# Performance work log

Hardware: AMD Instinct MI355X
Metric: run time of the kernel (lower is better)

Reference implementation:

```python
import jax, jax.numpy as jnp
import numpy as np

L, H, FF, NH = 6, 1024, 4096, 8
HD = H // NH
B, S = 4, 1024
EPS = 1e-5


def _fp8_roundtrip(w):
    # matches torch path: cast to float8_e4m3fn and back (done once at init, no grad)
    return w.astype(jnp.float8_e4m3fn).astype(w.dtype)


def setup_inputs() -> dict:
    key = jax.random.key(0)
    ks = jax.random.split(key, 6)
    x = jax.random.normal(ks[0], (B, S, H), dtype=jnp.float32)
    sH = 1.0 / np.sqrt(H)
    sF = 1.0 / np.sqrt(FF)
    qkv_w = _fp8_roundtrip(jax.random.normal(ks[1], (L, 3 * H, H), jnp.float32) * sH)
    proj_w = _fp8_roundtrip(jax.random.normal(ks[2], (L, H, H), jnp.float32) * sH)
    fc1_w = _fp8_roundtrip(jax.random.normal(ks[3], (L, FF, H), jnp.float32) * sH)
    fc2_w = _fp8_roundtrip(jax.random.normal(ks[4], (L, H, FF), jnp.float32) * sF)
    return {
        "x": x,
        "qkv_w": qkv_w, "qkv_b": jnp.zeros((L, 3 * H), jnp.float32),
        "proj_w": proj_w, "proj_b": jnp.zeros((L, H), jnp.float32),
        "fc1_w": fc1_w, "fc1_b": jnp.zeros((L, FF), jnp.float32),
        "fc2_w": fc2_w, "fc2_b": jnp.zeros((L, H), jnp.float32),
        "ln1_s": jnp.ones((L, H), jnp.float32), "ln1_b": jnp.zeros((L, H), jnp.float32),
        "ln2_s": jnp.ones((L, H), jnp.float32), "ln2_b": jnp.zeros((L, H), jnp.float32),
    }


def _layernorm(x, scale, bias):
    mu = jnp.mean(x, axis=-1, keepdims=True)
    var = jnp.var(x, axis=-1, keepdims=True)
    return (x - mu) / jnp.sqrt(var + EPS) * scale + bias


def reference(x, qkv_w, qkv_b, proj_w, proj_b, fc1_w, fc1_b, fc2_w, fc2_b,
              ln1_s, ln1_b, ln2_s, ln2_b):
    b, s, h = x.shape
    for i in range(L):
        # --- attention block ---
        residual = x
        hx = _layernorm(x, ln1_s[i], ln1_b[i])
        qkv = hx @ qkv_w[i].T + qkv_b[i]                       # [b, s, 3h]
        q, k, v = jnp.split(qkv, 3, axis=-1)
        q = q.reshape(b, s, NH, HD).transpose(0, 2, 1, 3)      # [b, nh, s, hd]
        k = k.reshape(b, s, NH, HD).transpose(0, 2, 1, 3)
        v = v.reshape(b, s, NH, HD).transpose(0, 2, 1, 3)
        scores = jnp.einsum('bhqd,bhkd->bhqk', q, k) / np.sqrt(HD)
        attn = jax.nn.softmax(scores, axis=-1)
        out = jnp.einsum('bhqk,bhkd->bhqd', attn, v)           # [b, nh, s, hd]
        out = out.transpose(0, 2, 1, 3).reshape(b, s, h)
        x = out @ proj_w[i].T + proj_b[i] + residual
        # --- FFN block ---
        residual = x
        hx = _layernorm(x, ln2_s[i], ln2_b[i])
        ff = jax.nn.relu(hx @ fc1_w[i].T + fc1_b[i])
        x = ff @ fc2_w[i].T + fc2_b[i] + residual
    return x
```

## Files before the change

kernel.cpp:

```cpp
#include <hip/hip_runtime.h>
#include <stdint.h>

typedef __bf16 bf16;
typedef __bf16 bf16x4 __attribute__((ext_vector_type(4)));
typedef __bf16 bf16x8 __attribute__((ext_vector_type(8)));
typedef float  f32x4  __attribute__((ext_vector_type(4)));

#define NLAYER 6
#define HDIM   1024
#define FFDIM  4096
#define NHEAD  8
#define HEADD  128
#define SEQ    1024
#define NTOK   4096

__device__ __forceinline__ void g2l16(const void* g, void* l) {
  __builtin_amdgcn_global_load_lds(
      (const __attribute__((address_space(1))) void*)g,
      (__attribute__((address_space(3))) void*)l, 16, 0, 0);
}

__global__ __launch_bounds__(256) void cvt_w(const float* __restrict__ in,
                                             bf16* __restrict__ out, int n8) {
  int i = blockIdx.x * 256 + threadIdx.x;
  if (i >= n8) return;
  const f32x4* p = (const f32x4*)in + (size_t)i * 2;
  f32x4 a = p[0], b = p[1];
  bf16x8 o;
  o[0] = (bf16)a[0]; o[1] = (bf16)a[1]; o[2] = (bf16)a[2]; o[3] = (bf16)a[3];
  o[4] = (bf16)b[0]; o[5] = (bf16)b[1]; o[6] = (bf16)b[2]; o[7] = (bf16)b[3];
  *((bf16x8*)out + i) = o;
}

__global__ __launch_bounds__(256) void ln_k(const float* __restrict__ x,
                                            const float* __restrict__ sc,
                                            const float* __restrict__ bi,
                                            bf16* __restrict__ out) {
  int row = blockIdx.x, t = threadIdx.x;
  f32x4 v = *((const f32x4*)(x + (size_t)row * HDIM) + t);
  float s = v[0] + v[1] + v[2] + v[3];
  float q = v[0]*v[0] + v[1]*v[1] + v[2]*v[2] + v[3]*v[3];
#pragma unroll
  for (int m = 1; m < 64; m <<= 1) {
    s += __shfl_xor(s, m, 64);
    q += __shfl_xor(q, m, 64);
  }
  __shared__ float ss[4], qq[4];
  if ((t & 63) == 0) { ss[t >> 6] = s; qq[t >> 6] = q; }
  __syncthreads();
  s = ss[0] + ss[1] + ss[2] + ss[3];
  q = qq[0] + qq[1] + qq[2] + qq[3];
  float mu  = s * (1.f / HDIM);
  float var = q * (1.f / HDIM) - mu * mu;
  float rs  = rsqrtf(var + 1e-5f);
  f32x4 g = *((const f32x4*)sc + t);
  f32x4 b = *((const f32x4*)bi + t);
  bf16x4 o;
#pragma unroll
  for (int j = 0; j < 4; j++) o[j] = (bf16)((v[j] - mu) * rs * g[j] + b[j]);
  *((bf16x4*)(out + (size_t)row * HDIM) + t) = o;
}

__global__ __launch_bounds__(256) void init_k(const float* __restrict__ resid,
                                              const float* __restrict__ bias,
                                              float* __restrict__ out) {
  int i = blockIdx.x * 256 + threadIdx.x;
  f32x4 b = *((const f32x4*)bias + (i & 255));
  f32x4 v = *((const f32x4*)resid + i);
  *((f32x4*)out + i) = v + b;
}

template <int SPLIT, bool RELU, bool RESID, bool OUTF32, bool SPLITV>
__global__ __launch_bounds__(256) void gemm_sb(const bf16* __restrict__ A,
                                               const bf16* __restrict__ W,
                                               const float* __restrict__ bias,
                                               const float* resid, void* outp,
                                               bf16* __restrict__ vt,
                                               int N, int K) {
  __shared__ bf16 As[128 * 64];
  __shared__ bf16 Bs[128 * 64];
  int tid = threadIdx.x;
  int lane = tid & 63, w = tid >> 6;
  int g = lane >> 4, r = lane & 15;
  int wr = w >> 1, wc = w & 1;
  int nbx = N >> 7;
  int cpx = gridDim.x >> 3;
  int swz = (blockIdx.x & 7) * cpx + (blockIdx.x >> 3);
  int bm = swz / nbx, bn = swz % nbx;
  const bf16* Ab = A + (size_t)bm * 128 * K;
  const bf16* Wb = W + (size_t)bn * 128 * K;
  f32x4 acc[4][4] = {};

  int Ksub = K / SPLIT;
  int kbase = (SPLIT > 1) ? (int)blockIdx.y * Ksub : 0;
  int nt = Ksub >> 6;

  for (int t = 0; t < nt; ++t) {
    int k0 = kbase + (t << 6);
#pragma unroll
    for (int i = 0; i < 4; ++i) {
      int c = i * 256 + tid;
      int row = c >> 3;
      int kk = ((c & 7) ^ (row & 7)) << 3;
      g2l16(Ab + (size_t)row * K + k0 + kk, (char*)As + c * 16);
      g2l16(Wb + (size_t)row * K + k0 + kk, (char*)Bs + c * 16);
    }
    __syncthreads();
#pragma unroll
    for (int ks = 0; ks < 2; ++ks) {
      bf16x8 af[4], bfr[4];
#pragma unroll
      for (int mi = 0; mi < 4; mi++) {
        int row = wr * 64 + mi * 16 + r;
        af[mi] = *(const bf16x8*)((const char*)As + row * 128 +
                                  ((ks * 64 + g * 16) ^ ((row & 7) << 4)));
      }
#pragma unroll
      for (int ni = 0; ni < 4; ni++) {
        int row = wc * 64 + ni * 16 + r;
        bfr[ni] = *(const bf16x8*)((const char*)Bs + row * 128 +
                                   ((ks * 64 + g * 16) ^ ((row & 7) << 4)));
      }
      __builtin_amdgcn_s_setprio(1);
#pragma unroll
      for (int mi = 0; mi < 4; mi++)
#pragma unroll
        for (int ni = 0; ni < 4; ni++)
          acc[mi][ni] = __builtin_amdgcn_mfma_f32_16x16x32_bf16(
              af[mi], bfr[ni], acc[mi][ni], 0, 0, 0);
      __builtin_amdgcn_s_setprio(0);
    }
    __syncthreads();
  }

#pragma unroll
  for (int ni = 0; ni < 4; ++ni) {
    int cbase = bn * 128 + wc * 64 + ni * 16;
    int col = cbase + r;
    if constexpr (SPLIT > 1) {
#pragma unroll
      for (int mi = 0; mi < 4; ++mi) {
        int row0 = bm * 128 + wr * 64 + mi * 16 + g * 4;
#pragma unroll
        for (int j = 0; j < 4; j++)
          unsafeAtomicAdd((float*)outp + (size_t)(row0 + j) * N + col,
                          acc[mi][ni][j]);
      }
    } else {
      float bv = bias[col];
      bool vpart = SPLITV && cbase >= 2048;
      if (vpart) {
        int hh = (col - 2048) >> 7, dd = col & 127;
#pragma unroll
        for (int mi = 0; mi < 4; ++mi) {
          int row0 = bm * 128 + wr * 64 + mi * 16 + g * 4;
          int bb = row0 >> 10, ss = row0 & 1023;
          bf16x4 o;
#pragma unroll
          for (int j = 0; j < 4; j++) o[j] = (bf16)(acc[mi][ni][j] + bv);
          *(bf16x4*)(vt + ((size_t)((bb * NHEAD + hh) * HEADD + dd)) * SEQ + ss) = o;
        }
      } else {
#pragma unroll
        for (int mi = 0; mi < 4; ++mi) {
          int row0 = bm * 128 + wr * 64 + mi * 16 + g * 4;
#pragma unroll
          for (int j = 0; j < 4; j++) {
            size_t idx = (size_t)(row0 + j) * N + col;
            float v = acc[mi][ni][j] + bv;
            if constexpr (RELU) v = fmaxf(v, 0.f);
            if constexpr (RESID) v += resid[idx];
            if constexpr (OUTF32) ((float*)outp)[idx] = v;
            else                  ((bf16*)outp)[idx] = (bf16)v;
          }
        }
      }
    }
  }
}

__global__ __launch_bounds__(256) void attn_k(const bf16* __restrict__ qkv,
                                              const bf16* __restrict__ vt,
                                              bf16* __restrict__ out) {
  __shared__ bf16 Ks[64 * 128];
  __shared__ bf16 VT[128 * 64];
  __shared__ bf16 Ps[4][1024];
  int qt = blockIdx.x, h = blockIdx.y, b = blockIdx.z;
  int tid = threadIdx.x, lane = tid & 63, w = tid >> 6;
  int g = lane >> 4, r = lane & 15;
  int q0 = qt * 64;
  size_t tok0 = (size_t)b * SEQ;
  char* psw = (char*)Ps + w * 2048;

  bf16x8 qf[4];
  {
    const bf16* qp = qkv + (tok0 + q0 + w * 16 + r) * 3072 + h * HEADD;
#pragma unroll
    for (int ks = 0; ks < 4; ks++) qf[ks] = *(const bf16x8*)(qp + ks * 32 + g * 8);
  }
  f32x4 oacc[8] = {};
  float mprev[4], lsum[4];
#pragma unroll
  for (int j = 0; j < 4; j++) { mprev[j] = -1e30f; lsum[j] = 0.f; }
  const float scl = 0.08838834764831845f;
  const bf16* vtb = vt + (size_t)(b * NHEAD + h) * HEADD * SEQ;

  for (int c0 = 0; c0 < SEQ; c0 += 64) {
    const bf16* kbase = qkv + (tok0 + c0) * 3072 + 1024 + h * HEADD;
#pragma unroll
    for (int i = 0; i < 4; i++) {
      int cb = i * 256 + w * 64;
      int c  = cb + lane;
      int krow = c >> 4;
      int kkk  = ((c & 15) ^ (krow & 7)) << 3;
      g2l16(kbase + (size_t)krow * 3072 + kkk, (char*)Ks + cb * 16);
      int vrow = c >> 3;
      int vcol = ((c & 7) ^ (vrow & 7)) << 3;
      g2l16(vtb + (size_t)vrow * SEQ + c0 + vcol, (char*)VT + cb * 16);
    }
    __syncthreads();

    f32x4 sacc[4] = {};
#pragma unroll
    for (int ks = 0; ks < 4; ks++) {
#pragma unroll
      for (int cb = 0; cb < 4; cb++) {
        int row = cb * 16 + r;
        bf16x8 kf = *(const bf16x8*)((const char*)Ks + row * 256 +
                                     ((ks * 64 + g * 16) ^ ((row & 7) << 4)));
        sacc[cb] = __builtin_amdgcn_mfma_f32_16x16x32_bf16(qf[ks], kf, sacc[cb], 0, 0, 0);
      }
    }
#pragma unroll
    for (int cb = 0; cb < 4; cb++) {
      sacc[cb][0] *= scl; sacc[cb][1] *= scl; sacc[cb][2] *= scl; sacc[cb][3] *= scl;
    }
    float sf[4];
#pragma unroll
    for (int j = 0; j < 4; j++) {
      float m = fmaxf(fmaxf(sacc[0][j], sacc[1][j]), fmaxf(sacc[2][j], sacc[3][j]));
      m = fmaxf(m, __shfl_xor(m, 1, 64));
      m = fmaxf(m, __shfl_xor(m, 2, 64));
      m = fmaxf(m, __shfl_xor(m, 4, 64));
      m = fmaxf(m, __shfl_xor(m, 8, 64));
      float mn = fmaxf(mprev[j], m);
      float f  = __expf(mprev[j] - mn);
      mprev[j] = mn; sf[j] = f;
      float rs = 0.f;
#pragma unroll
      for (int cb = 0; cb < 4; cb++) {
        float p = __expf(sacc[cb][j] - mn);
        sacc[cb][j] = p; rs += p;
      }
      rs += __shfl_xor(rs, 1, 64);
      rs += __shfl_xor(rs, 2, 64);
      rs += __shfl_xor(rs, 4, 64);
      rs += __shfl_xor(rs, 8, 64);
      lsum[j] = lsum[j] * f + rs;
    }
#pragma unroll
    for (int nb = 0; nb < 8; nb++) {
      oacc[nb][0] *= sf[0]; oacc[nb][1] *= sf[1];
      oacc[nb][2] *= sf[2]; oacc[nb][3] *= sf[3];
    }
#pragma unroll
    for (int cb = 0; cb < 4; cb++) {
      int cbyte = cb * 32 + r * 2;
#pragma unroll
      for (int j = 0; j < 4; j++) {
        int q = g * 4 + j;
        *(bf16*)(psw + q * 128 + (cbyte ^ ((q & 7) << 4))) = (bf16)sacc[cb][j];
      }
    }
    asm volatile("s_waitcnt lgkmcnt(0)" ::: "memory");
    __builtin_amdgcn_sched_barrier(0);
#pragma unroll
    for (int cs = 0; cs < 2; cs++) {
      bf16x8 pf = *(const bf16x8*)(psw + r * 128 + ((cs * 64 + g * 16) ^ ((r & 7) << 4)));
#pragma unroll
      for (int nb = 0; nb < 8; nb++) {
        int vrow = nb * 16 + r;
        bf16x8 vf = *(const bf16x8*)((const char*)VT + vrow * 128 +
                                     ((cs * 64 + g * 16) ^ ((vrow & 7) << 4)));
        oacc[nb] = __builtin_amdgcn_mfma_f32_16x16x32_bf16(pf, vf, oacc[nb], 0, 0, 0);
      }
    }
    __syncthreads();
  }

  float rl[4];
#pragma unroll
  for (int j = 0; j < 4; j++) rl[j] = 1.f / lsum[j];
#pragma unroll
  for (int nb = 0; nb < 8; nb++)
#pragma unroll
    for (int j = 0; j < 4; j++)
      out[(tok0 + q0 + w * 16 + g * 4 + j) * HDIM + h * HEADD + nb * 16 + r] =
          (bf16)(oacc[nb][j] * rl[j]);
}

extern "C" void kernel_launch(void* const* d_in, const int* in_sizes, int n_in,
                              void* d_out, int out_size, void* d_ws, size_t ws_size,
                              hipStream_t stream) {
  const float* x_in   = (const float*)d_in[0];
  const float* qkv_w  = (const float*)d_in[1];
  const float* qkv_b  = (const float*)d_in[2];
  const float* proj_w = (const float*)d_in[3];
  const float* proj_b = (const float*)d_in[4];
  const float* fc1_w  = (const float*)d_in[5];
  const float* fc1_b  = (const float*)d_in[6];
  const float* fc2_w  = (const float*)d_in[7];
  const float* fc2_b  = (const float*)d_in[8];
  const float* ln1_s  = (const float*)d_in[9];
  const float* ln1_b  = (const float*)d_in[10];
  const float* ln2_s  = (const float*)d_in[11];
  const float* ln2_b  = (const float*)d_in[12];

  char* ws = (char*)d_ws;
  size_t o = 0;
  bf16* Wq = (bf16*)(ws + o); o += (size_t)NLAYER * 3 * HDIM * HDIM * 2;
  bf16* Wp = (bf16*)(ws + o); o += (size_t)NLAYER * HDIM * HDIM * 2;
  bf16* W1 = (bf16*)(ws + o); o += (size_t)NLAYER * FFDIM * HDIM * 2;
  bf16* W2 = (bf16*)(ws + o); o += (size_t)NLAYER * HDIM * FFDIM * 2;
  bf16* hx   = (bf16*)(ws + o); o += (size_t)NTOK * HDIM * 2;
  bf16* qkvb = (bf16*)(ws + o); o += (size_t)NTOK * 3 * HDIM * 2;
  bf16* Vt   = (bf16*)(ws + o); o += (size_t)NTOK * HDIM * 2;
  bf16* aout = (bf16*)(ws + o); o += (size_t)NTOK * HDIM * 2;
  bf16* ffb  = (bf16*)(ws + o); o += (size_t)NTOK * FFDIM * 2;
  float* xbuf = (float*)d_out;

  {
    int n8;
    n8 = NLAYER * 3 * HDIM * HDIM / 8;
    cvt_w<<<(n8 + 255) / 256, 256, 0, stream>>>(qkv_w, Wq, n8);
    n8 = NLAYER * HDIM * HDIM / 8;
    cvt_w<<<(n8 + 255) / 256, 256, 0, stream>>>(proj_w, Wp, n8);
    n8 = NLAYER * FFDIM * HDIM / 8;
    cvt_w<<<(n8 + 255) / 256, 256, 0, stream>>>(fc1_w, W1, n8);
    n8 = NLAYER * HDIM * FFDIM / 8;
    cvt_w<<<(n8 + 255) / 256, 256, 0, stream>>>(fc2_w, W2, n8);
  }

  const int initg = NTOK * HDIM / 4 / 256;

  for (int i = 0; i < NLAYER; i++) {
    const float* xc = (i == 0) ? x_in : xbuf;
    ln_k<<<NTOK, 256, 0, stream>>>(xc, ln1_s + i * HDIM, ln1_b + i * HDIM, hx);
    gemm_sb<1, false, false, false, true>
        <<<(NTOK / 128) * (3 * HDIM / 128), 256, 0, stream>>>(
        hx, Wq + (size_t)i * 3 * HDIM * HDIM, qkv_b + i * 3 * HDIM, nullptr,
        qkvb, Vt, 3 * HDIM, HDIM);
    attn_k<<<dim3(SEQ / 64, NHEAD, 4), 256, 0, stream>>>(qkvb, Vt, aout);
    init_k<<<initg, 256, 0, stream>>>(xc, proj_b + i * HDIM, xbuf);
    gemm_sb<4, false, false, true, false>
        <<<dim3((NTOK / 128) * (HDIM / 128), 4), 256, 0, stream>>>(
        aout, Wp + (size_t)i * HDIM * HDIM, nullptr, nullptr,
        xbuf, nullptr, HDIM, HDIM);
    ln_k<<<NTOK, 256, 0, stream>>>(xbuf, ln2_s + i * HDIM, ln2_b + i * HDIM, hx);
    gemm_sb<1, true, false, false, false>
        <<<(NTOK / 128) * (FFDIM / 128), 256, 0, stream>>>(
        hx, W1 + (size_t)i * FFDIM * HDIM, fc1_b + i * FFDIM, nullptr,
        ffb, nullptr, FFDIM, HDIM);
    init_k<<<initg, 256, 0, stream>>>(xbuf, fc2_b + i * HDIM, xbuf);
    gemm_sb<4, false, false, true, false>
        <<<dim3((NTOK / 128) * (HDIM / 128), 4), 256, 0, stream>>>(
        ffb, W2 + (size_t)i * HDIM * FFDIM, nullptr, nullptr,
        xbuf, nullptr, HDIM, FFDIM);
  }
  (void)in_sizes; (void)n_in; (void)out_size; (void)ws_size;
}
```

Measured before the change: 1.858 ms.

## Use 256x256 GEMM tiles with 512 threads and double-buffered LDS staging

Replaces the 128x128, 256-thread GEMM with a 256x256 tile computed by 8 waves. Each wave now holds an 8x4 set of 16x16 accumulators. LDS is double-buffered so the global-to-LDS loads for the next K slice are issued before computing the current one, which halves the barriers per K step. The larger tile raises arithmetic intensity per LDS and global byte. The costs are roughly 128KB of LDS per block (one block per CU), heavier register use, and far fewer blocks: the QKV GEMM launches only 192 blocks, which may leave CUs idle.

```diff
diff --git a/kernel.cpp b/kernel.cpp
--- a/kernel.cpp
+++ b/kernel.cpp
@@ -71,76 +71,86 @@
 }
 
 template <int SPLIT, bool RELU, bool RESID, bool OUTF32, bool SPLITV>
-__global__ __launch_bounds__(256) void gemm_sb(const bf16* __restrict__ A,
+__global__ __launch_bounds__(512) void gemm256(const bf16* __restrict__ A,
                                                const bf16* __restrict__ W,
                                                const float* __restrict__ bias,
                                                const float* resid, void* outp,
                                                bf16* __restrict__ vt,
                                                int N, int K) {
-  __shared__ bf16 As[128 * 64];
-  __shared__ bf16 Bs[128 * 64];
+  __shared__ bf16 As[2][256 * 64];
+  __shared__ bf16 Bs[2][256 * 64];
   int tid = threadIdx.x;
   int lane = tid & 63, w = tid >> 6;
   int g = lane >> 4, r = lane & 15;
-  int wr = w >> 1, wc = w & 1;
-  int nbx = N >> 7;
+  int wr = w >> 2, wc = w & 3;
+  int nbx = N >> 8;
   int cpx = gridDim.x >> 3;
   int swz = (blockIdx.x & 7) * cpx + (blockIdx.x >> 3);
   int bm = swz / nbx, bn = swz % nbx;
-  const bf16* Ab = A + (size_t)bm * 128 * K;
-  const bf16* Wb = W + (size_t)bn * 128 * K;
-  f32x4 acc[4][4] = {};
-
-  int Ksub = K / SPLIT;
-  int kbase = (SPLIT > 1) ? (int)blockIdx.y * Ksub : 0;
-  int nt = Ksub >> 6;
-
-  for (int t = 0; t < nt; ++t) {
-    int k0 = kbase + (t << 6);
+  const bf16* Ab = A + (size_t)bm * 256 * K;
+  const bf16* Wb = W + (size_t)bn * 256 * K;
+  f32x4 acc[8][4] = {};
+
+  auto STAGE = [&](int buf, int k0) {
 #pragma unroll
     for (int i = 0; i < 4; ++i) {
-      int c = i * 256 + tid;
+      int c = i * 512 + tid;
       int row = c >> 3;
       int kk = ((c & 7) ^ (row & 7)) << 3;
-      g2l16(Ab + (size_t)row * K + k0 + kk, (char*)As + c * 16);
-      g2l16(Wb + (size_t)row * K + k0 + kk, (char*)Bs + c * 16);
-    }
-    __syncthreads();
+      g2l16(Ab + (size_t)row * K + k0 + kk, (char*)As[buf] + c * 16);
+      g2l16(Wb + (size_t)row * K + k0 + kk, (char*)Bs[buf] + c * 16);
+    }
+  };
+  auto COMPUTE = [&](int buf) {
 #pragma unroll
     for (int ks = 0; ks < 2; ++ks) {
-      bf16x8 af[4], bfr[4];
-#pragma unroll
-      for (int mi = 0; mi < 4; mi++) {
-        int row = wr * 64 + mi * 16 + r;
-        af[mi] = *(const bf16x8*)((const char*)As + row * 128 +
+      bf16x8 af[8], bfr[4];
+#pragma unroll
+      for (int mi = 0; mi < 8; mi++) {
+        int row = wr * 128 + mi * 16 + r;
+        af[mi] = *(const bf16x8*)((const char*)As[buf] + row * 128 +
                                   ((ks * 64 + g * 16) ^ ((row & 7) << 4)));
       }
 #pragma unroll
       for (int ni = 0; ni < 4; ni++) {
         int row = wc * 64 + ni * 16 + r;
-        bfr[ni] = *(const bf16x8*)((const char*)Bs + row * 128 +
+        bfr[ni] = *(const bf16x8*)((const char*)Bs[buf] + row * 128 +
                                    ((ks * 64 + g * 16) ^ ((row & 7) << 4)));
       }
       __builtin_amdgcn_s_setprio(1);
 #pragma unroll
-      for (int mi = 0; mi < 4; mi++)
+      for (int mi = 0; mi < 8; mi++)
 #pragma unroll
         for (int ni = 0; ni < 4; ni++)
           acc[mi][ni] = __builtin_amdgcn_mfma_f32_16x16x32_bf16(
               af[mi], bfr[ni], acc[mi][ni], 0, 0, 0);
       __builtin_amdgcn_s_setprio(0);
     }
+  };
+
+  int Ksub = K / SPLIT;
+  int kbase = (SPLIT > 1) ? (int)blockIdx.y * Ksub : 0;
+  int nt = Ksub >> 6;
+
+  STAGE(0, kbase);
+  __syncthreads();
+  int cur = 0;
+  for (int t = 0; t < nt - 1; ++t) {
+    STAGE(cur ^ 1, kbase + ((t + 1) << 6));
+    COMPUTE(cur);
     __syncthreads();
-  }
+    cur ^= 1;
+  }
+  COMPUTE(cur);
 
 #pragma unroll
   for (int ni = 0; ni < 4; ++ni) {
-    int cbase = bn * 128 + wc * 64 + ni * 16;
+    int cbase = bn * 256 + wc * 64 + ni * 16;
     int col = cbase + r;
     if constexpr (SPLIT > 1) {
 #pragma unroll
-      for (int mi = 0; mi < 4; ++mi) {
-        int row0 = bm * 128 + wr * 64 + mi * 16 + g * 4;
+      for (int mi = 0; mi < 8; ++mi) {
+        int row0 = bm * 256 + wr * 128 + mi * 16 + g * 4;
 #pragma unroll
         for (int j = 0; j < 4; j++)
           unsafeAtomicAdd((float*)outp + (size_t)(row0 + j) * N + col,
@@ -152,8 +162,8 @@
       if (vpart) {
         int hh = (col - 2048) >> 7, dd = col & 127;
 #pragma unroll
-        for (int mi = 0; mi < 4; ++mi) {
-          int row0 = bm * 128 + wr * 64 + mi * 16 + g * 4;
+        for (int mi = 0; mi < 8; ++mi) {
+          int row0 = bm * 256 + wr * 128 + mi * 16 + g * 4;
           int bb = row0 >> 10, ss = row0 & 1023;
           bf16x4 o;
 #pragma unroll
@@ -162,8 +172,8 @@
         }
       } else {
 #pragma unroll
-        for (int mi = 0; mi < 4; ++mi) {
-          int row0 = bm * 128 + wr * 64 + mi * 16 + g * 4;
+        for (int mi = 0; mi < 8; ++mi) {
+          int row0 = bm * 256 + wr * 128 + mi * 16 + g * 4;
 #pragma unroll
           for (int j = 0; j < 4; j++) {
             size_t idx = (size_t)(row0 + j) * N + col;
@@ -346,24 +356,24 @@
   for (int i = 0; i < NLAYER; i++) {
     const float* xc = (i == 0) ? x_in : xbuf;
     ln_k<<<NTOK, 256, 0, stream>>>(xc, ln1_s + i * HDIM, ln1_b + i * HDIM, hx);
-    gemm_sb<1, false, false, false, true>
-        <<<(NTOK / 128) * (3 * HDIM / 128), 256, 0, stream>>>(
+    gemm256<1, false, false, false, true>
+        <<<(NTOK / 256) * (3 * HDIM / 256), 512, 0, stream>>>(
         hx, Wq + (size_t)i * 3 * HDIM * HDIM, qkv_b + i * 3 * HDIM, nullptr,
         qkvb, Vt, 3 * HDIM, HDIM);
     attn_k<<<dim3(SEQ / 64, NHEAD, 4), 256, 0, stream>>>(qkvb, Vt, aout);
     init_k<<<initg, 256, 0, stream>>>(xc, proj_b + i * HDIM, xbuf);
-    gemm_sb<4, false, false, true, false>
-        <<<dim3((NTOK / 128) * (HDIM / 128), 4), 256, 0, stream>>>(
+    gemm256<4, false, false, true, false>
+        <<<dim3((NTOK / 256) * (HDIM / 256), 4), 512, 0, stream>>>(
         aout, Wp + (size_t)i * HDIM * HDIM, nullptr, nullptr,
         xbuf, nullptr, HDIM, HDIM);
     ln_k<<<NTOK, 256, 0, stream>>>(xbuf, ln2_s + i * HDIM, ln2_b + i * HDIM, hx);
-    gemm_sb<1, true, false, false, false>
-        <<<(NTOK / 128) * (FFDIM / 128), 256, 0, stream>>>(
+    gemm256<1, true, false, false, false>
+        <<<(NTOK / 256) * (FFDIM / 256), 512, 0, stream>>>(
         hx, W1 + (size_t)i * FFDIM * HDIM, fc1_b + i * FFDIM, nullptr,
         ffb, nullptr, FFDIM, HDIM);
     init_k<<<initg, 256, 0, stream>>>(xbuf, fc2_b + i * HDIM, xbuf);
-    gemm_sb<4, false, false, true, false>
-        <<<dim3((NTOK / 128) * (HDIM / 128), 4), 256, 0, stream>>>(
+    gemm256<4, false, false, true, false>
+        <<<dim3((NTOK / 256) * (HDIM / 256), 4), 512, 0, stream>>>(
         ffb, W2 + (size_t)i * HDIM * FFDIM, nullptr, nullptr,
         xbuf, nullptr, HDIM, FFDIM);
   }
```

After: 1.927 ms. +3.7%, slower.
